# Performance work log

Hardware: AMD Instinct MI355X
Metric: run time of the kernel (lower is better)

The kernel has to match this reference:

```python
import jax, jax.numpy as jnp
import numpy as np

B, N, M, D, H = 2, 2048, 77, 1024, 16
DH = D // H
SCALE = DH ** -0.5
EPS = 1e-5


def _round_ste(x):
    return x + jax.lax.stop_gradient(jnp.round(x) - x)


def _fq(x, delta, zp, n_bits):
    # UniformAffineQuantizer: fake quant-dequant with straight-through round
    xi = _round_ste(x / delta) + zp
    xq = jnp.clip(xi, 0.0, 2.0 ** n_bits - 1.0)
    return (xq - zp) * delta


def _ln(x, g, b):
    mu = jnp.mean(x, -1, keepdims=True)
    var = jnp.var(x, -1, keepdims=True)
    return (x - mu) * jax.lax.rsqrt(var + EPS) * g + b


def _attn(x, ctx, wq, wk, wv, wo, bo, dq, dk, dv, dw):
    b, n, _ = x.shape
    m = ctx.shape[1]
    q = (x @ wq).reshape(b, n, H, DH).transpose(0, 2, 1, 3)   # b h n d
    k = (ctx @ wk).reshape(b, m, H, DH).transpose(0, 2, 1, 3)
    v = (ctx @ wv).reshape(b, m, H, DH).transpose(0, 2, 1, 3)
    sim = jnp.einsum('bhid,bhjd->bhij', _fq(q, dq, 128.0, 8), _fq(k, dk, 128.0, 8)) * SCALE
    attn = jax.nn.softmax(sim, axis=-1)
    out = jnp.einsum('bhij,bhjd->bhid', _fq(attn, dw, 0.0, 8), _fq(v, dv, 128.0, 8))
    out = out.transpose(0, 2, 1, 3).reshape(b, n, D)
    return out @ wo + bo


def setup_inputs():
    key = jax.random.key(0)
    ks = jax.random.split(key, 16)
    w = lambda k, s: (jax.random.normal(k, s, jnp.float32) * 0.02)
    d = lambda v: jnp.full((1,), v, jnp.float32)
    return {
        'x': jax.random.normal(ks[0], (B, N, D), jnp.float32),
        'context': jax.random.normal(ks[1], (B, M, D), jnp.float32),
        'ln1_g': jnp.ones((D,), jnp.float32), 'ln1_b': jnp.zeros((D,), jnp.float32),
        'ln2_g': jnp.ones((D,), jnp.float32), 'ln2_b': jnp.zeros((D,), jnp.float32),
        'ln3_g': jnp.ones((D,), jnp.float32), 'ln3_b': jnp.zeros((D,), jnp.float32),
        'a1_wq': w(ks[2], (D, D)), 'a1_wk': w(ks[3], (D, D)), 'a1_wv': w(ks[4], (D, D)),
        'a1_wo': w(ks[5], (D, D)), 'a1_bo': jnp.zeros((D,), jnp.float32),
        'a2_wq': w(ks[6], (D, D)), 'a2_wk': w(ks[7], (D, D)), 'a2_wv': w(ks[8], (D, D)),
        'a2_wo': w(ks[9], (D, D)), 'a2_bo': jnp.zeros((D,), jnp.float32),
        'ff_w1': w(ks[10], (D, 8 * D)), 'ff_b1': jnp.zeros((8 * D,), jnp.float32),
        'ff_w2': w(ks[11], (4 * D, D)), 'ff_b2': jnp.zeros((D,), jnp.float32),
        'd_q1': d(0.02), 'd_k1': d(0.02), 'd_v1': d(0.02), 'd_w1': d(1.0 / 255.0),
        'd_q2': d(0.02), 'd_k2': d(0.02), 'd_v2': d(0.02), 'd_w2': d(1.0 / 255.0),
    }


def reference(x, context, ln1_g, ln1_b, ln2_g, ln2_b, ln3_g, ln3_b,
              a1_wq, a1_wk, a1_wv, a1_wo, a1_bo,
              a2_wq, a2_wk, a2_wv, a2_wo, a2_bo,
              ff_w1, ff_b1, ff_w2, ff_b2,
              d_q1, d_k1, d_v1, d_w1, d_q2, d_k2, d_v2, d_w2):
    # x = attn1(norm1(x)) + x   (self-attention)
    h1 = _ln(x, ln1_g, ln1_b)
    x = _attn(h1, h1, a1_wq, a1_wk, a1_wv, a1_wo, a1_bo, d_q1, d_k1, d_v1, d_w1) + x
    # x = attn2(norm2(x), context) + x   (cross-attention)
    h2 = _ln(x, ln2_g, ln2_b)
    x = _attn(h2, context, a2_wq, a2_wk, a2_wv, a2_wo, a2_bo, d_q2, d_k2, d_v2, d_w2) + x
    # x = ff(norm3(x)) + x   (GEGLU feed-forward)
    h3 = _ln(x, ln3_g, ln3_b)
    hg = h3 @ ff_w1 + ff_b1
    a, g = jnp.split(hg, 2, axis=-1)
    x = (a * jax.nn.gelu(g, approximate=False)) @ ff_w2 + ff_b2 + x
    return x
```

## Files before the change

### kernel.cpp

```cpp
#include <hip/hip_runtime.h>
#include <cstdint>
#include <cmath>

typedef unsigned short u16;
typedef unsigned int   u32;

typedef __bf16 bx8 __attribute__((ext_vector_type(8)));
typedef float  fx4 __attribute__((ext_vector_type(4)));

#define H_  16
#define DH_ 64
#define QSCALE 0.18033688011112042f

__device__ __forceinline__ float bf2f(u16 h){ return __uint_as_float(((u32)h) << 16); }
__device__ __forceinline__ u16 f2bf(float f){
  u32 u = __float_as_uint(f);
  u32 r = (u + 0x7FFFu + ((u >> 16) & 1u)) >> 16;
  return (u16)r;
}

__device__ __forceinline__ u32 pk_bf16(float a, float b){
  u32 r;
  asm("v_cvt_pk_bf16_f32 %0, %1, %2" : "=v"(r) : "v"(a), "v"(b));
  return r;
}

__device__ __forceinline__ float ldv(const void* p, size_t i, int f32){
  return f32 ? ((const float*)p)[i] : bf2f(((const u16*)p)[i]);
}

__device__ __forceinline__ void gld16(const void* g, void* l){
  __builtin_amdgcn_global_load_lds((const __attribute__((address_space(1))) u32*)g,
                                   (__attribute__((address_space(3))) u32*)l,
                                   16, 0, 0);
}

__device__ __forceinline__ float fq_val(float v, float delta){
  float xi = rintf(v / delta) + 128.0f;
  xi = fminf(fmaxf(xi, 0.0f), 255.0f);
  return (xi - 128.0f) * delta;
}

__device__ __forceinline__ float gelu_f(float x){
  float x3 = x * x * x;
  float z = 0.7978845608028654f * x + 0.035677408136300125f * x3;
  float u = __expf(-2.0f * z);
  float t = 1.0f - 2.0f * u / (1.0f + u);
  return 0.5f * x * (1.0f + t);
}

__global__ void detect_k(const u32* __restrict__ x, int* __restrict__ flag){
  __shared__ int cnt;
  if (threadIdx.x == 0) cnt = 0;
  __syncthreads();
  u32 w = x[threadIdx.x];
  int e = (w >> 7) & 0xFF;
  if (e >= 100 && e <= 140) atomicAdd(&cnt, 1);
  __syncthreads();
  if (threadIdx.x == 0) *flag = (cnt < 192) ? 1 : 0;
}

__global__ __launch_bounds__(256) void cvt_k(const void* __restrict__ in, u16* __restrict__ out,
                                             int n, const int* __restrict__ flagp){
  int f32 = *flagp;
  int i = blockIdx.x * 256 + threadIdx.x;
  if (i < n) out[i] = f32 ? f2bf(((const float*)in)[i]) : ((const u16*)in)[i];
}

__global__ __launch_bounds__(256) void tr8_k(
    const void* s0, const void* s1, const void* s2, const void* s3,
    const void* s4, const void* s5, const void* s6, const void* s7,
    u16* __restrict__ out, const int* __restrict__ flagp){
  __shared__ u16 t[32][33];
  int f32 = *flagp;
  int z = blockIdx.z;
  const void* in = z==0?s0:z==1?s1:z==2?s2:z==3?s3:z==4?s4:z==5?s5:z==6?s6:s7;
  u16* o = out + ((size_t)z << 20);
  int n0 = blockIdx.x << 5, r0 = blockIdx.y << 5;
  int tx = threadIdx.x & 31, ty = threadIdx.x >> 5;
  #pragma unroll
  for (int i = 0; i < 4; i++)
    t[ty + i*8][tx] = f2bf(ldv(in, (size_t)(r0 + ty + i*8) * 1024 + n0 + tx, f32));
  __syncthreads();
  #pragma unroll
  for (int i = 0; i < 4; i++)
    o[(size_t)(n0 + ty + i*8) * 1024 + r0 + tx] = t[tx][ty + i*8];
}

__global__ __launch_bounds__(256) void tr_k(const void* __restrict__ in, u16* __restrict__ out,
                                            int Rout, int C, const int* __restrict__ flagp){
  __shared__ u16 t[32][33];
  int f32 = *flagp;
  int n0 = blockIdx.x << 5, r0 = blockIdx.y << 5;
  int tx = threadIdx.x & 31, ty = threadIdx.x >> 5;
  #pragma unroll
  for (int i = 0; i < 4; i++)
    t[ty + i*8][tx] = f2bf(ldv(in, (size_t)(r0 + ty + i*8) * C + n0 + tx, f32));
  __syncthreads();
  #pragma unroll
  for (int i = 0; i < 4; i++)
    out[(size_t)(n0 + ty + i*8) * Rout + r0 + tx] = t[tx][ty + i*8];
}

__global__ __launch_bounds__(256) void ln_k(const void* __restrict__ x,
    const void* __restrict__ gam, const void* __restrict__ bet, u16* __restrict__ out,
    const int* __restrict__ flagp, int xdual){
  __shared__ float sb[8];
  const int f32 = *flagp;
  const int f32x = xdual ? f32 : 0;
  const int row = blockIdx.x, t = threadIdx.x;
  float v0, v1, v2, v3;
  if (f32x){
    float4 xv = *(const float4*)((const float*)x + (size_t)row * 1024 + t * 4);
    v0 = xv.x; v1 = xv.y; v2 = xv.z; v3 = xv.w;
  } else {
    ushort4 xv = *(const ushort4*)((const u16*)x + (size_t)row * 1024 + t * 4);
    v0 = bf2f(xv.x); v1 = bf2f(xv.y); v2 = bf2f(xv.z); v3 = bf2f(xv.w);
  }
  float s = v0 + v1 + v2 + v3;
  #pragma unroll
  for (int mk = 32; mk; mk >>= 1) s += __shfl_xor(s, mk);
  if ((t & 63) == 0) sb[t >> 6] = s;
  __syncthreads();
  float mu = (sb[0] + sb[1] + sb[2] + sb[3]) * 0.0009765625f;
  float d0 = v0 - mu, d1 = v1 - mu, d2 = v2 - mu, d3 = v3 - mu;
  float ss = d0*d0 + d1*d1 + d2*d2 + d3*d3;
  #pragma unroll
  for (int mk = 32; mk; mk >>= 1) ss += __shfl_xor(ss, mk);
  if ((t & 63) == 0) sb[4 + (t >> 6)] = ss;
  __syncthreads();
  float var = (sb[4] + sb[5] + sb[6] + sb[7]) * 0.0009765625f;
  float rs = rsqrtf(var + 1e-5f);
  int c = t * 4;
  u16 o0 = f2bf(d0 * rs * ldv(gam, c+0, f32) + ldv(bet, c+0, f32));
  u16 o1 = f2bf(d1 * rs * ldv(gam, c+1, f32) + ldv(bet, c+1, f32));
  u16 o2 = f2bf(d2 * rs * ldv(gam, c+2, f32) + ldv(bet, c+2, f32));
  u16 o3 = f2bf(d3 * rs * ldv(gam, c+3, f32) + ldv(bet, c+3, f32));
  uint2 ov; ov.x = (u32)o0 | ((u32)o1 << 16); ov.y = (u32)o2 | ((u32)o3 << 16);
  *(uint2*)(out + (size_t)row * 1024 + c) = ov;
}

__global__ __launch_bounds__(512)
void gemm_mr(const u16* __restrict__ A, const u16* __restrict__ BT,
             u16* __restrict__ P0, u16* __restrict__ P1, u16* __restrict__ P2,
             const void* D0, const void* D1, const void* D2,
             float sc0, float sc1, float sc2,
             int md0, int md1, int md2,
             const int* __restrict__ flagp,
             int M, int K, int rpb, int npad)
{
  __shared__ u16 As[2][128 * 32];
  __shared__ u16 Bs[2][128 * 32];
  const int tid = threadIdx.x;
  const int l = tid & 63, w = tid >> 6;
  const int lr = l & 15, lq = l >> 4;
  const int m0 = blockIdx.y * 128, n0 = blockIdx.x * 128;
  const int wrow = (w & 3) * 32, wcol = (w >> 2) * 64;

  fx4 acc[2][4];
  #pragma unroll
  for (int i = 0; i < 2; i++)
    #pragma unroll
    for (int j = 0; j < 4; j++){ fx4 z = {0.f,0.f,0.f,0.f}; acc[i][j] = z; }

  const int r0 = tid >> 2, p0 = tid & 3;
  const int c0 = p0 ^ (r0 & 3);
  int am0 = m0 + r0; if (am0 > M - 1) am0 = M - 1;
  const u16* gA = A  + (size_t)am0 * K + c0 * 8;
  const u16* gB = BT + (size_t)(n0 + r0) * K + c0 * 8;
  const int lo = w * 512;

  const int nk = K >> 5;
  gld16(gA, &As[0][lo]);
  gld16(gB, &Bs[0][lo]);

  for (int kt = 0; kt < nk; ++kt){
    __syncthreads();
    const int cur = kt & 1;
    if (kt + 1 < nk){
      const int nb = cur ^ 1;
      const int ko = (kt + 1) << 5;
      gld16(gA + ko, &As[nb][lo]);
      gld16(gB + ko, &Bs[nb][lo]);
    }
    bx8 aF[2], bF[4];
    #pragma unroll
    for (int i = 0; i < 2; i++){
      int row = wrow + i * 16 + lr;
      aF[i] = *(const bx8*)&As[cur][row * 32 + (lq ^ (row & 3)) * 8];
    }
    #pragma unroll
    for (int j = 0; j < 4; j++){
      int row = wcol + j * 16 + lr;
      bF[j] = *(const bx8*)&Bs[cur][row * 32 + (lq ^ (row & 3)) * 8];
    }
    #pragma unroll
    for (int i = 0; i < 2; i++)
      #pragma unroll
      for (int j = 0; j < 4; j++)
        acc[i][j] = __builtin_amdgcn_mfma_f32_16x16x32_bf16(aF[i], bF[j], acc[i][j], 0, 0, 0);
  }

  const int f32 = *flagp;
  const int reg = n0 >> 10;
  const int cbase = n0 & 1023;
  u16* P = reg == 0 ? P0 : (reg == 1 ? P1 : P2);
  const void* D = reg == 0 ? D0 : (reg == 1 ? D1 : D2);
  const float sc = reg == 0 ? sc0 : (reg == 1 ? sc1 : sc2);
  const int md = reg == 0 ? md0 : (reg == 1 ? md1 : md2);
  const float delta = ldv(D, 0, f32);

  #pragma unroll
  for (int i = 0; i < 2; i++)
    #pragma unroll
    for (int j = 0; j < 4; j++)
      #pragma unroll
      for (int rr = 0; rr < 4; rr++){
        int gm = m0 + wrow + i * 16 + lq * 4 + rr;
        int col = cbase + wcol + j * 16 + lr;
        if (gm < M){
          float v = fq_val(acc[i][j][rr], delta) * sc;
          if (md == 0){
            P[(size_t)gm * 1024 + col] = f2bf(v);
          } else {
            int bb = gm / rpb; int jj = gm - bb * rpb;
            int hh = col >> 6, dh = col & 63;
            P[(size_t)((bb * H_ + hh) * DH_ + dh) * npad + jj] = f2bf(v);
          }
        }
      }
}

template<int MODE>
__global__ __launch_bounds__(256)
void gemm64(const u16* __restrict__ A, const u16* __restrict__ BT,
            void* __restrict__ Co, const void* __restrict__ res,
            const void* __restrict__ bias, const void* __restrict__ dptr, float sc,
            const int* __restrict__ flagp, int res_dual,
            int M, int K)
{
  __shared__ u16 As[2][64 * 32];
  __shared__ u16 Bs[2][128 * 32];
  const int tid = threadIdx.x;
  const int l = tid & 63, w = tid >> 6;
  const int lr = l & 15, lq = l >> 4;
  const int m0 = blockIdx.y * 64, n0 = blockIdx.x * 128;
  const int wrow = (w >> 1) * 32, wcol = (w & 1) * 64;

  fx4 acc[2][4];
  #pragma unroll
  for (int i = 0; i < 2; i++)
    #pragma unroll
    for (int j = 0; j < 4; j++){ fx4 z = {0.f,0.f,0.f,0.f}; acc[i][j] = z; }

  const int r0 = tid >> 2, p0 = tid & 3;
  const int c0 = p0 ^ (r0 & 3);
  const int r1 = r0 + 64;
  int am0 = m0 + r0; if (am0 > M - 1) am0 = M - 1;
  const u16* gA0 = A  + (size_t)am0 * K + c0 * 8;
  const u16* gB0 = BT + (size_t)(n0 + r0) * K + c0 * 8;
  const u16* gB1 = BT + (size_t)(n0 + r1) * K + c0 * 8;
  const int lo0 = (w * 64) * 8, lo1 = (256 + w * 64) * 8;

  const int nk = K >> 5;
  gld16(gA0, &As[0][lo0]);
  gld16(gB0, &Bs[0][lo0]);
  gld16(gB1, &Bs[0][lo1]);

  for (int kt = 0; kt < nk; ++kt){
    __syncthreads();
    const int cur = kt & 1;
    if (kt + 1 < nk){
      const int nb = cur ^ 1;
      const int ko = (kt + 1) << 5;
      gld16(gA0 + ko, &As[nb][lo0]);
      gld16(gB0 + ko, &Bs[nb][lo0]);
      gld16(gB1 + ko, &Bs[nb][lo1]);
    }
    bx8 aF[2], bF[4];
    #pragma unroll
    for (int i = 0; i < 2; i++){
      int row = wrow + i * 16 + lr;
      aF[i] = *(const bx8*)&As[cur][row * 32 + (lq ^ (row & 3)) * 8];
    }
    #pragma unroll
    for (int j = 0; j < 4; j++){
      int row = wcol + j * 16 + lr;
      bF[j] = *(const bx8*)&Bs[cur][row * 32 + (lq ^ (row & 3)) * 8];
    }
    #pragma unroll
    for (int i = 0; i < 2; i++)
      #pragma unroll
      for (int j = 0; j < 4; j++)
        acc[i][j] = __builtin_amdgcn_mfma_f32_16x16x32_bf16(aF[i], bF[j], acc[i][j], 0, 0, 0);
  }

  const int f32 = *flagp;
  float delta = 1.f;
  if (MODE == 0) delta = ldv(dptr, 0, f32);

  #pragma unroll
  for (int i = 0; i < 2; i++)
    #pragma unroll
    for (int j = 0; j < 4; j++)
      #pragma unroll
      for (int rr = 0; rr < 4; rr++){
        int gm = m0 + wrow + i * 16 + lq * 4 + rr;
        int gn = n0 + wcol + j * 16 + lr;
        if (gm < M){
          float v = acc[i][j][rr];
          size_t idx = (size_t)gm * 1024 + gn;
          if (MODE == 0){
            ((u16*)Co)[idx] = f2bf(fq_val(v, delta) * sc);
          } else if (MODE == 5){
            float r = res_dual ? ldv(res, idx, f32) : bf2f(((const u16*)res)[idx]);
            ((u16*)Co)[idx] = f2bf(v + ldv(bias, gn, f32) + r);
          } else {
            float o = v + ldv(bias, gn, f32) + bf2f(((const u16*)res)[idx]);
            if (f32) ((float*)Co)[idx] = o;
            else     ((u16*)Co)[idx]  = f2bf(o);
          }
        }
      }
}

__global__ __launch_bounds__(512)
void gemm_glu(const u16* __restrict__ A, const u16* __restrict__ WT,
              u16* __restrict__ GE, const void* __restrict__ bias,
              const int* __restrict__ flagp, int M, int K)
{
  __shared__ u16 As[2][128 * 32];
  __shared__ u16 Ba[2][128 * 32];
  __shared__ u16 Bg[2][128 * 32];
  const int tid = threadIdx.x;
  const int l = tid & 63, w = tid >> 6;
  const int lr = l & 15, lq = l >> 4;
  const int m0 = blockIdx.y * 128, n0 = blockIdx.x * 128;
  const int wrow = (w & 3) * 32, wcol = (w >> 2) * 64;

  fx4 accA[2][4], accG[2][4];
  #pragma unroll
  for (int i = 0; i < 2; i++)
    #pragma unroll
    for (int j = 0; j < 4; j++){
      fx4 z = {0.f,0.f,0.f,0.f}; accA[i][j] = z; accG[i][j] = z;
    }

  const int r0 = tid >> 2, p0 = tid & 3;
  const int c0 = p0 ^ (r0 & 3);
  int am0 = m0 + r0; if (am0 > M - 1) am0 = M - 1;
  const u16* gA  = A  + (size_t)am0 * K + c0 * 8;
  const u16* gBa = WT + (size_t)(n0 + r0) * K + c0 * 8;
  const u16* gBg = WT + (size_t)(4096 + n0 + r0) * K + c0 * 8;
  const int lo = w * 512;

  const int nk = K >> 5;
  gld16(gA,  &As[0][lo]);
  gld16(gBa, &Ba[0][lo]);
  gld16(gBg, &Bg[0][lo]);

  for (int kt = 0; kt < nk; ++kt){
    __syncthreads();
    const int cur = kt & 1;
    if (kt + 1 < nk){
      const int nb = cur ^ 1;
      const int ko = (kt + 1) << 5;
      gld16(gA + ko,  &As[nb][lo]);
      gld16(gBa + ko, &Ba[nb][lo]);
      gld16(gBg + ko, &Bg[nb][lo]);
    }
    bx8 aF[2], bFa[4], bFg[4];
    #pragma unroll
    for (int i = 0; i < 2; i++){
      int row = wrow + i * 16 + lr;
      aF[i] = *(const bx8*)&As[cur][row * 32 + (lq ^ (row & 3)) * 8];
    }
    #pragma unroll
    for (int j = 0; j < 4; j++){
      int row = wcol + j * 16 + lr;
      bFa[j] = *(const bx8*)&Ba[cur][row * 32 + (lq ^ (row & 3)) * 8];
      bFg[j] = *(const bx8*)&Bg[cur][row * 32 + (lq ^ (row & 3)) * 8];
    }
    #pragma unroll
    for (int i = 0; i < 2; i++)
      #pragma unroll
      for (int j = 0; j < 4; j++){
        accA[i][j] = __builtin_amdgcn_mfma_f32_16x16x32_bf16(aF[i], bFa[j], accA[i][j], 0, 0, 0);
        accG[i][j] = __builtin_amdgcn_mfma_f32_16x16x32_bf16(aF[i], bFg[j], accG[i][j], 0, 0, 0);
      }
  }

  const int f32 = *flagp;

  #pragma unroll
  for (int i = 0; i < 2; i++)
    #pragma unroll
    for (int j = 0; j < 4; j++)
      #pragma unroll
      for (int rr = 0; rr < 4; rr++){
        int gm = m0 + wrow + i * 16 + lq * 4 + rr;
        int gn = n0 + wcol + j * 16 + lr;
        float va = accA[i][j][rr] + ldv(bias, gn, f32);
        float vg = accG[i][j][rr] + ldv(bias, 4096 + gn, f32);
        GE[(size_t)gm * 4096 + gn] = f2bf(va * gelu_f(vg));
      }
}

__global__ __launch_bounds__(512, 4) void attn_k(
    const u16* __restrict__ Qf, const u16* __restrict__ Kf,
    const u16* __restrict__ VT, u16* __restrict__ AO,
    const void* __restrict__ dwp, const int* __restrict__ flagp,
    int Nq, int Lk, int Lpad)
{
  __shared__ u16 lds[40960];
  u16* const KB0 = lds;
  u16* const KB1 = lds + 8192;
  u16* const Vs  = lds + 16384;
  u16* const Ps  = lds + 24576;

  const int tid = threadIdx.x, l = tid & 63, w = tid >> 6;
  const int lr = l & 15, lq = l >> 4, m = lr & 7;
  const int q0 = blockIdx.x << 7;
  const int b = blockIdx.y >> 4, hh = blockIdx.y & 15;
  const int wq = w << 4;
  const float dw = ldv(dwp, 0, *flagp);

  const u16* qp = Qf + ((size_t)(b * Nq + q0 + wq + lr) << 10) + (hh << 6) + (lq << 3);
  bx8 aQ0 = *(const bx8*)(qp);
  bx8 aQ1 = *(const bx8*)(qp + 32);

  const int krl = (w << 3) + (l >> 3), kcl = l & 7;
  const int vrl = (w << 2) + (l >> 4), vcl = l & 15;

  auto stageK = [&](u16* dst, int j0){
    #pragma unroll
    for (int t = 0; t < 2; ++t){
      int r = krl + (t << 6);
      int jr = j0 + r; if (jr > Lk - 1) jr = Lk - 1;
      int c = kcl ^ (r & 7);
      gld16(Kf + ((size_t)(b * Lk + jr) << 10) + (hh << 6) + (c << 3),
            dst + (w << 9) + (t << 12));
    }
  };
  auto stageV = [&](int j0){
    #pragma unroll
    for (int t = 0; t < 2; ++t){
      int dh = vrl + (t << 5);
      int c = vcl ^ (dh & 7);
      gld16(VT + (size_t)((((b << 4) + hh) << 6) + dh) * Lpad + j0 + (c << 3),
            Vs + (w << 9) + (t << 12));
    }
  };

  const int ntiles = (Lk + 127) >> 7;
  const int ch0 = ((lq ^ m) << 3), ch1 = (((lq + 4) ^ m) << 3);

  float sa0 = 0.f, sa1 = 0.f, sa2 = 0.f, sa3 = 0.f;
  stageK(KB0, 0);
  for (int jt = 0; jt < ntiles; ++jt){
    __syncthreads();
    const u16* Kc = (jt & 1) ? KB1 : KB0;
    if (jt + 1 < ntiles) stageK((jt & 1) ? KB0 : KB1, (jt + 1) << 7);
    const int j0 = jt << 7;
    const bool full = (j0 + 128 <= Lk);
    #pragma unroll
    for (int j = 0; j < 8; ++j){
      const int ro = ((j << 4) + lr) << 6;
      bx8 k0 = *(const bx8*)&Kc[ro + ch0];
      bx8 k1 = *(const bx8*)&Kc[ro + ch1];
      fx4 sv = {0.f,0.f,0.f,0.f};
      sv = __builtin_amdgcn_mfma_f32_16x16x32_bf16(k0, aQ0, sv, 0, 0, 0);
      sv = __builtin_amdgcn_mfma_f32_16x16x32_bf16(k1, aQ1, sv, 0, 0, 0);
      if (full){
        sa0 += exp2f(sv[0]); sa1 += exp2f(sv[1]);
        sa2 += exp2f(sv[2]); sa3 += exp2f(sv[3]);
      } else {
        const int kb = j0 + (j << 4) + (lq << 2);
        sa0 += (kb + 0 < Lk) ? exp2f(sv[0]) : 0.f;
        sa1 += (kb + 1 < Lk) ? exp2f(sv[1]) : 0.f;
        sa2 += (kb + 2 < Lk) ? exp2f(sv[2]) : 0.f;
        sa3 += (kb + 3 < Lk) ? exp2f(sv[3]) : 0.f;
      }
    }
  }
  __syncthreads();
  float s = (sa0 + sa1) + (sa2 + sa3);
  s += __shfl_xor(s, 16);
  s += __shfl_xor(s, 32);
  const float cr = (1.0f / dw) / s;

  fx4 oacc[4];
  #pragma unroll
  for (int dj = 0; dj < 4; ++dj){ fx4 z = {0.f,0.f,0.f,0.f}; oacc[dj] = z; }

  const int qloc = wq + lr;
  const int pw = (qloc << 7) + (lq << 2);

  stageK(KB0, 0);
  for (int jt = 0; jt < ntiles; ++jt){
    __syncthreads();
    const int j0 = jt << 7;
    stageV(j0);
    if (jt + 1 < ntiles) stageK((jt & 1) ? KB0 : KB1, j0 + 128);
    const u16* Kc = (jt & 1) ? KB1 : KB0;
    const bool full = (j0 + 128 <= Lk);
    #pragma unroll
    for (int j = 0; j < 8; ++j){
      const int ro = ((j << 4) + lr) << 6;
      bx8 k0 = *(const bx8*)&Kc[ro + ch0];
      bx8 k1 = *(const bx8*)&Kc[ro + ch1];
      fx4 sv = {0.f,0.f,0.f,0.f};
      sv = __builtin_amdgcn_mfma_f32_16x16x32_bf16(k0, aQ0, sv, 0, 0, 0);
      sv = __builtin_amdgcn_mfma_f32_16x16x32_bf16(k1, aQ1, sv, 0, 0, 0);
      float x0, x1, x2, x3;
      if (full){
        x0 = rintf(exp2f(sv[0]) * cr);
        x1 = rintf(exp2f(sv[1]) * cr);
        x2 = rintf(exp2f(sv[2]) * cr);
        x3 = rintf(exp2f(sv[3]) * cr);
      } else {
        const int kb = j0 + (j << 4) + (lq << 2);
        x0 = (kb + 0 < Lk) ? rintf(exp2f(sv[0]) * cr) : 0.f;
        x1 = (kb + 1 < Lk) ? rintf(exp2f(sv[1]) * cr) : 0.f;
        x2 = (kb + 2 < Lk) ? rintf(exp2f(sv[2]) * cr) : 0.f;
        x3 = (kb + 3 < Lk) ? rintf(exp2f(sv[3]) * cr) : 0.f;
      }
      uint2 pp; pp.x = pk_bf16(x0, x1); pp.y = pk_bf16(x2, x3);
      *(uint2*)&Ps[pw + ((j ^ m) << 4)] = pp;
    }
    __syncthreads();
    #pragma unroll
    for (int kk = 0; kk < 4; ++kk){
      bx8 aP = *(const bx8*)&Ps[(qloc << 7) + ((((kk << 3) + (lq << 1)) ^ (m << 2)) << 2)];
      #pragma unroll
      for (int dj = 0; dj < 4; ++dj){
        bx8 bV = *(const bx8*)&Vs[((((dj << 4) + lr)) << 7) + ((((kk << 2) + lq) ^ m) << 3)];
        oacc[dj] = __builtin_amdgcn_mfma_f32_16x16x32_bf16(aP, bV, oacc[dj], 0, 0, 0);
      }
    }
  }

  const size_t ob = ((size_t)(b * Nq + q0 + wq + (lq << 2)) << 10) + (hh << 6) + lr;
  #pragma unroll
  for (int dj = 0; dj < 4; ++dj)
    #pragma unroll
    for (int rr = 0; rr < 4; ++rr)
      AO[ob + ((size_t)rr << 10) + (dj << 4)] = f2bf(oacc[dj][rr] * dw);
}


extern "C" void kernel_launch(void* const* d_in, const int* in_sizes, int n_in,
                              void* d_out, int out_size, void* d_ws, size_t ws_size,
                              hipStream_t stream)
{
  const void* X    = d_in[0];
  const void* CTX  = d_in[1];
  const void* LN1G = d_in[2];
  const void* LN1B = d_in[3];
  const void* LN2G = d_in[4];
  const void* LN2B = d_in[5];
  const void* LN3G = d_in[6];
  const void* LN3B = d_in[7];
  const void* W1Q  = d_in[8];
  const void* W1K  = d_in[9];
  const void* W1V  = d_in[10];
  const void* W1O  = d_in[11];
  const void* B1O  = d_in[12];
  const void* W2Q  = d_in[13];
  const void* W2K  = d_in[14];
  const void* W2V  = d_in[15];
  const void* W2O  = d_in[16];
  const void* B2O  = d_in[17];
  const void* FW1  = d_in[18];
  const void* FB1  = d_in[19];
  const void* FW2  = d_in[20];
  const void* FB2  = d_in[21];
  const void* DQ1  = d_in[22];
  const void* DK1  = d_in[23];
  const void* DV1  = d_in[24];
  const void* DW1  = d_in[25];
  const void* DQ2  = d_in[26];
  const void* DK2  = d_in[27];
  const void* DV2  = d_in[28];
  const void* DW2  = d_in[29];

  char* ws = (char*)d_ws;
  u16* wslot = (u16*)(ws + (0ull  << 20));
  u16* xs    = (u16*)(ws + (16ull << 20));
  u16* h     = (u16*)(ws + (24ull << 20));
  u16* bufA  = (u16*)(ws + (32ull << 20));
  u16* bufB  = (u16*)(ws + (40ull << 20));
  u16* bufC  = (u16*)(ws + (48ull << 20));
  u16* ge    = bufA;
  u16* ctxc  = (u16*)(ws + (64ull << 20));
  int* flag  = (int*)(ws + (65ull << 20));

  const dim3 G8x64(8, 64), GAT(16, 32);
  const int NCTX = 154 * 1024;
  const size_t MB2 = 1048576;

  detect_k<<<1, 256, 0, stream>>>((const u32*)X, flag);
  cvt_k<<<(NCTX + 255) / 256, 256, 0, stream>>>(CTX, ctxc, NCTX, flag);
  tr8_k<<<dim3(32, 32, 8), 256, 0, stream>>>(W1Q, W1K, W1V, W1O, W2Q, W2K, W2V, W2O,
                                             wslot, flag);

  ln_k<<<4096, 256, 0, stream>>>(X, LN1G, LN1B, h, flag, 1);
  gemm_mr<<<dim3(24, 32), 512, 0, stream>>>(h, wslot,
      bufA, bufB, bufC, DQ1, DK1, DV1, QSCALE, 1.f, 1.f, 0, 0, 1,
      flag, 4096, 1024, 2048, 2048);
  attn_k<<<GAT, 512, 0, stream>>>(bufA, bufB, bufC, h, DW1, flag, 2048, 2048, 2048);
  gemm64<5><<<G8x64, 256, 0, stream>>>(h, wslot + 3 * MB2, xs, X, B1O, nullptr, 1.f,
                                       flag, 1, 4096, 1024);

  ln_k<<<4096, 256, 0, stream>>>(xs, LN2G, LN2B, h, flag, 0);
  gemm64<0><<<G8x64, 256, 0, stream>>>(h, wslot + 4 * MB2, bufA, nullptr, nullptr, DQ2,
                                       QSCALE, flag, 0, 4096, 1024);
  gemm_mr<<<dim3(16, 2), 512, 0, stream>>>(ctxc, wslot + 5 * MB2,
      bufB, bufC, nullptr, DK2, DV2, DV2, 1.f, 1.f, 1.f, 0, 1, 1,
      flag, 154, 1024, 77, 128);
  attn_k<<<GAT, 512, 0, stream>>>(bufA, bufB, bufC, h, DW2, flag, 2048, 77, 128);
  gemm64<5><<<G8x64, 256, 0, stream>>>(h, wslot + 7 * MB2, xs, xs, B2O, nullptr, 1.f,
                                       flag, 0, 4096, 1024);

  ln_k<<<4096, 256, 0, stream>>>(xs, LN3G, LN3B, h, flag, 0);
  tr_k<<<dim3(256, 32), 256, 0, stream>>>(FW1, wslot, 1024, 8192, flag);
  gemm_glu<<<dim3(32, 32), 512, 0, stream>>>(h, wslot, ge, FB1, flag, 4096, 1024);
  tr_k<<<dim3(32, 128), 256, 0, stream>>>(FW2, wslot, 4096, 1024, flag);
  gemm64<7><<<G8x64, 256, 0, stream>>>(ge, wslot, d_out, xs, FB2, nullptr, 1.f,
                                       flag, 0, 4096, 4096);
}
```

Baseline: 659.2 us.

## Restructure attention kernel: 4 waves with 32 query rows, register P via permlane

The attention kernel now runs 256 threads per block, and each wave handles two 16-row query groups. Each K fragment loaded from LDS is therefore reused across two MFMA chains. The P matrix no longer goes through an LDS round trip and barrier: the accumulators are computed transposed and repacked in registers with permlane swap instructions. V is also double-buffered alongside K, which removes the mid-tile barrier, and exp2 uses the hardware intrinsic. This costs more registers per wave and lowers the wave count per block, which may reduce latency hiding.

```diff
diff --git a/kernel.cpp b/kernel.cpp
--- a/kernel.cpp
+++ b/kernel.cpp
@@ -7,10 +7,17 @@
 
 typedef __bf16 bx8 __attribute__((ext_vector_type(8)));
 typedef float  fx4 __attribute__((ext_vector_type(4)));
+typedef u32    ux4 __attribute__((ext_vector_type(4)));
 
 #define H_  16
 #define DH_ 64
 #define QSCALE 0.18033688011112042f
+
+#if __has_builtin(__builtin_amdgcn_exp2f)
+#define EXP2(x) __builtin_amdgcn_exp2f(x)
+#else
+#define EXP2(x) exp2f(x)
+#endif
 
 __device__ __forceinline__ float bf2f(u16 h){ return __uint_as_float(((u32)h) << 16); }
 __device__ __forceinline__ u16 f2bf(float f){
@@ -24,6 +31,8 @@
   asm("v_cvt_pk_bf16_f32 %0, %1, %2" : "=v"(r) : "v"(a), "v"(b));
   return r;
 }
+
+union pkc { ux4 u; bx8 v; };
 
 __device__ __forceinline__ float ldv(const void* p, size_t i, int f32){
   return f32 ? ((const float*)p)[i] : bf2f(((const u16*)p)[i]);
@@ -406,61 +415,72 @@
       }
 }
 
-__global__ __launch_bounds__(512, 4) void attn_k(
+__global__ __launch_bounds__(256) void attn_k(
     const u16* __restrict__ Qf, const u16* __restrict__ Kf,
     const u16* __restrict__ VT, u16* __restrict__ AO,
     const void* __restrict__ dwp, const int* __restrict__ flagp,
     int Nq, int Lk, int Lpad)
 {
-  __shared__ u16 lds[40960];
-  u16* const KB0 = lds;
-  u16* const KB1 = lds + 8192;
-  u16* const Vs  = lds + 16384;
-  u16* const Ps  = lds + 24576;
+  __shared__ u16 lds[32768];
+  u16* const KB0_ = lds;
+  u16* const KB1_ = lds + 8192;
+  u16* const VB0_ = lds + 16384;
+  u16* const VB1_ = lds + 24576;
 
   const int tid = threadIdx.x, l = tid & 63, w = tid >> 6;
   const int lr = l & 15, lq = l >> 4, m = lr & 7;
   const int q0 = blockIdx.x << 7;
   const int b = blockIdx.y >> 4, hh = blockIdx.y & 15;
-  const int wq = w << 4;
+  const int wq = w << 5;
   const float dw = ldv(dwp, 0, *flagp);
-
-  const u16* qp = Qf + ((size_t)(b * Nq + q0 + wq + lr) << 10) + (hh << 6) + (lq << 3);
-  bx8 aQ0 = *(const bx8*)(qp);
-  bx8 aQ1 = *(const bx8*)(qp + 32);
-
-  const int krl = (w << 3) + (l >> 3), kcl = l & 7;
-  const int vrl = (w << 2) + (l >> 4), vcl = l & 15;
+  const float rdw = 1.0f / dw;
+
+  bx8 aQ[2][2];
+  #pragma unroll
+  for (int g = 0; g < 2; ++g){
+    const u16* qp = Qf + ((size_t)(b * Nq + q0 + wq + g * 16 + lr) << 10)
+                       + (hh << 6) + (lq << 3);
+    aQ[g][0] = *(const bx8*)(qp);
+    aQ[g][1] = *(const bx8*)(qp + 32);
+  }
+
+  const int kr0 = tid >> 3, kc = (tid & 7) ^ (kr0 & 7);
+  const int vd0 = tid >> 4, vc = (tid & 15) ^ (vd0 & 7);
+  const int ldsb = w << 9;
 
   auto stageK = [&](u16* dst, int j0){
     #pragma unroll
-    for (int t = 0; t < 2; ++t){
-      int r = krl + (t << 6);
+    for (int q = 0; q < 4; ++q){
+      int r = kr0 + (q << 5);
       int jr = j0 + r; if (jr > Lk - 1) jr = Lk - 1;
-      int c = kcl ^ (r & 7);
-      gld16(Kf + ((size_t)(b * Lk + jr) << 10) + (hh << 6) + (c << 3),
-            dst + (w << 9) + (t << 12));
+      gld16(Kf + ((size_t)(b * Lk + jr) << 10) + (hh << 6) + (kc << 3),
+            dst + (q << 11) + ldsb);
     }
   };
-  auto stageV = [&](int j0){
-    #pragma unroll
-    for (int t = 0; t < 2; ++t){
-      int dh = vrl + (t << 5);
-      int c = vcl ^ (dh & 7);
-      gld16(VT + (size_t)((((b << 4) + hh) << 6) + dh) * Lpad + j0 + (c << 3),
-            Vs + (w << 9) + (t << 12));
+  auto stageV = [&](u16* dst, int j0){
+    #pragma unroll
+    for (int q = 0; q < 4; ++q){
+      int d = vd0 + (q << 4);
+      gld16(VT + ((size_t)(((b << 4) + hh) << 6) + d) * Lpad + j0 + (vc << 3),
+            dst + (q << 11) + ldsb);
     }
   };
 
   const int ntiles = (Lk + 127) >> 7;
   const int ch0 = ((lq ^ m) << 3), ch1 = (((lq + 4) ^ m) << 3);
 
-  float sa0 = 0.f, sa1 = 0.f, sa2 = 0.f, sa3 = 0.f;
-  stageK(KB0, 0);
+  float sa[2][4];
+  #pragma unroll
+  for (int g = 0; g < 2; ++g)
+    #pragma unroll
+    for (int rr = 0; rr < 4; ++rr) sa[g][rr] = 0.f;
+
+  stageK(KB0_, 0);
   for (int jt = 0; jt < ntiles; ++jt){
     __syncthreads();
-    const u16* Kc = (jt & 1) ? KB1 : KB0;
-    if (jt + 1 < ntiles) stageK((jt & 1) ? KB0 : KB1, (jt + 1) << 7);
+    const int cur = jt & 1;
+    if (jt + 1 < ntiles) stageK(cur ? KB0_ : KB1_, (jt + 1) << 7);
+    const u16* Kc = cur ? KB1_ : KB0_;
     const int j0 = jt << 7;
     const bool full = (j0 + 128 <= Lk);
     #pragma unroll
@@ -468,84 +488,117 @@
       const int ro = ((j << 4) + lr) << 6;
       bx8 k0 = *(const bx8*)&Kc[ro + ch0];
       bx8 k1 = *(const bx8*)&Kc[ro + ch1];
-      fx4 sv = {0.f,0.f,0.f,0.f};
-      sv = __builtin_amdgcn_mfma_f32_16x16x32_bf16(k0, aQ0, sv, 0, 0, 0);
-      sv = __builtin_amdgcn_mfma_f32_16x16x32_bf16(k1, aQ1, sv, 0, 0, 0);
-      if (full){
-        sa0 += exp2f(sv[0]); sa1 += exp2f(sv[1]);
-        sa2 += exp2f(sv[2]); sa3 += exp2f(sv[3]);
-      } else {
-        const int kb = j0 + (j << 4) + (lq << 2);
-        sa0 += (kb + 0 < Lk) ? exp2f(sv[0]) : 0.f;
-        sa1 += (kb + 1 < Lk) ? exp2f(sv[1]) : 0.f;
-        sa2 += (kb + 2 < Lk) ? exp2f(sv[2]) : 0.f;
-        sa3 += (kb + 3 < Lk) ? exp2f(sv[3]) : 0.f;
-      }
-    }
-  }
+      #pragma unroll
+      for (int g = 0; g < 2; ++g){
+        fx4 sv = {0.f,0.f,0.f,0.f};
+        sv = __builtin_amdgcn_mfma_f32_16x16x32_bf16(k0, aQ[g][0], sv, 0, 0, 0);
+        sv = __builtin_amdgcn_mfma_f32_16x16x32_bf16(k1, aQ[g][1], sv, 0, 0, 0);
+        if (full){
+          sa[g][0] += EXP2(sv[0]); sa[g][1] += EXP2(sv[1]);
+          sa[g][2] += EXP2(sv[2]); sa[g][3] += EXP2(sv[3]);
+        } else {
+          const int kb = j0 + (j << 4) + (lq << 2);
+          sa[g][0] += (kb + 0 < Lk) ? EXP2(sv[0]) : 0.f;
+          sa[g][1] += (kb + 1 < Lk) ? EXP2(sv[1]) : 0.f;
+          sa[g][2] += (kb + 2 < Lk) ? EXP2(sv[2]) : 0.f;
+          sa[g][3] += (kb + 3 < Lk) ? EXP2(sv[3]) : 0.f;
+        }
+      }
+    }
+  }
+
+  float cr[2];
+  #pragma unroll
+  for (int g = 0; g < 2; ++g){
+    float s = (sa[g][0] + sa[g][1]) + (sa[g][2] + sa[g][3]);
+    s += __shfl_xor(s, 16);
+    s += __shfl_xor(s, 32);
+    cr[g] = rdw / s;
+  }
+
+  fx4 oacc[2][4];
+  #pragma unroll
+  for (int g = 0; g < 2; ++g)
+    #pragma unroll
+    for (int dj = 0; dj < 4; ++dj){ fx4 z = {0.f,0.f,0.f,0.f}; oacc[g][dj] = z; }
+
   __syncthreads();
-  float s = (sa0 + sa1) + (sa2 + sa3);
-  s += __shfl_xor(s, 16);
-  s += __shfl_xor(s, 32);
-  const float cr = (1.0f / dw) / s;
-
-  fx4 oacc[4];
-  #pragma unroll
-  for (int dj = 0; dj < 4; ++dj){ fx4 z = {0.f,0.f,0.f,0.f}; oacc[dj] = z; }
-
-  const int qloc = wq + lr;
-  const int pw = (qloc << 7) + (lq << 2);
-
-  stageK(KB0, 0);
+  stageK(KB0_, 0);
+  stageV(VB0_, 0);
   for (int jt = 0; jt < ntiles; ++jt){
     __syncthreads();
+    const int cur = jt & 1;
     const int j0 = jt << 7;
-    stageV(j0);
-    if (jt + 1 < ntiles) stageK((jt & 1) ? KB0 : KB1, j0 + 128);
-    const u16* Kc = (jt & 1) ? KB1 : KB0;
+    if (jt + 1 < ntiles){
+      stageK(cur ? KB0_ : KB1_, j0 + 128);
+      stageV(cur ? VB0_ : VB1_, j0 + 128);
+    }
+    const u16* Kc = cur ? KB1_ : KB0_;
+    const u16* Vc = cur ? VB1_ : VB0_;
     const bool full = (j0 + 128 <= Lk);
     #pragma unroll
-    for (int j = 0; j < 8; ++j){
-      const int ro = ((j << 4) + lr) << 6;
-      bx8 k0 = *(const bx8*)&Kc[ro + ch0];
-      bx8 k1 = *(const bx8*)&Kc[ro + ch1];
-      fx4 sv = {0.f,0.f,0.f,0.f};
-      sv = __builtin_amdgcn_mfma_f32_16x16x32_bf16(k0, aQ0, sv, 0, 0, 0);
-      sv = __builtin_amdgcn_mfma_f32_16x16x32_bf16(k1, aQ1, sv, 0, 0, 0);
-      float x0, x1, x2, x3;
-      if (full){
-        x0 = rintf(exp2f(sv[0]) * cr);
-        x1 = rintf(exp2f(sv[1]) * cr);
-        x2 = rintf(exp2f(sv[2]) * cr);
-        x3 = rintf(exp2f(sv[3]) * cr);
-      } else {
-        const int kb = j0 + (j << 4) + (lq << 2);
-        x0 = (kb + 0 < Lk) ? rintf(exp2f(sv[0]) * cr) : 0.f;
-        x1 = (kb + 1 < Lk) ? rintf(exp2f(sv[1]) * cr) : 0.f;
-        x2 = (kb + 2 < Lk) ? rintf(exp2f(sv[2]) * cr) : 0.f;
-        x3 = (kb + 3 < Lk) ? rintf(exp2f(sv[3]) * cr) : 0.f;
-      }
-      uint2 pp; pp.x = pk_bf16(x0, x1); pp.y = pk_bf16(x2, x3);
-      *(uint2*)&Ps[pw + ((j ^ m) << 4)] = pp;
-    }
-    __syncthreads();
-    #pragma unroll
-    for (int kk = 0; kk < 4; ++kk){
-      bx8 aP = *(const bx8*)&Ps[(qloc << 7) + ((((kk << 3) + (lq << 1)) ^ (m << 2)) << 2)];
+    for (int t = 0; t < 4; ++t){
+      u32 pA0[2], pA1[2], pB0[2], pB1[2];
+      #pragma unroll
+      for (int jj = 0; jj < 2; ++jj){
+        const int j = (t << 1) + jj;
+        const int ro = ((j << 4) + lr) << 6;
+        bx8 k0 = *(const bx8*)&Kc[ro + ch0];
+        bx8 k1 = *(const bx8*)&Kc[ro + ch1];
+        #pragma unroll
+        for (int g = 0; g < 2; ++g){
+          fx4 sv = {0.f,0.f,0.f,0.f};
+          sv = __builtin_amdgcn_mfma_f32_16x16x32_bf16(k0, aQ[g][0], sv, 0, 0, 0);
+          sv = __builtin_amdgcn_mfma_f32_16x16x32_bf16(k1, aQ[g][1], sv, 0, 0, 0);
+          float x0, x1, x2, x3;
+          if (full){
+            x0 = rintf(EXP2(sv[0]) * cr[g]);
+            x1 = rintf(EXP2(sv[1]) * cr[g]);
+            x2 = rintf(EXP2(sv[2]) * cr[g]);
+            x3 = rintf(EXP2(sv[3]) * cr[g]);
+          } else {
+            const int kb = j0 + (j << 4) + (lq << 2);
+            x0 = (kb + 0 < Lk) ? rintf(EXP2(sv[0]) * cr[g]) : 0.f;
+            x1 = (kb + 1 < Lk) ? rintf(EXP2(sv[1]) * cr[g]) : 0.f;
+            x2 = (kb + 2 < Lk) ? rintf(EXP2(sv[2]) * cr[g]) : 0.f;
+            x3 = (kb + 3 < Lk) ? rintf(EXP2(sv[3]) * cr[g]) : 0.f;
+          }
+          u32 plo = pk_bf16(x0, x1), phi = pk_bf16(x2, x3);
+          if (jj == 0){ pA0[g] = plo; pA1[g] = phi; }
+          else        { pB0[g] = plo; pB1[g] = phi; }
+        }
+      }
+      bx8 pa[2];
+      #pragma unroll
+      for (int g = 0; g < 2; ++g){
+        u32 r0 = pA0[g], r2 = pB0[g], r1 = pA1[g], r3 = pB1[g];
+        asm volatile("v_permlane32_swap_b32 %0, %1" : "+v"(r0), "+v"(r2));
+        asm volatile("v_permlane16_swap_b32 %0, %1" : "+v"(r0), "+v"(r2));
+        asm volatile("v_permlane32_swap_b32 %0, %1" : "+v"(r1), "+v"(r3));
+        asm volatile("v_permlane16_swap_b32 %0, %1" : "+v"(r1), "+v"(r3));
+        pkc pc; ux4 uu = {r0, r1, r2, r3}; pc.u = uu; pa[g] = pc.v;
+      }
       #pragma unroll
       for (int dj = 0; dj < 4; ++dj){
-        bx8 bV = *(const bx8*)&Vs[((((dj << 4) + lr)) << 7) + ((((kk << 2) + lq) ^ m) << 3)];
-        oacc[dj] = __builtin_amdgcn_mfma_f32_16x16x32_bf16(aP, bV, oacc[dj], 0, 0, 0);
-      }
-    }
-  }
-
-  const size_t ob = ((size_t)(b * Nq + q0 + wq + (lq << 2)) << 10) + (hh << 6) + lr;
-  #pragma unroll
-  for (int dj = 0; dj < 4; ++dj)
-    #pragma unroll
-    for (int rr = 0; rr < 4; ++rr)
-      AO[ob + ((size_t)rr << 10) + (dj << 4)] = f2bf(oacc[dj][rr] * dw);
+        bx8 bV = *(const bx8*)&Vc[(((dj << 4) + lr) << 7) + ((((t << 2) + lq) ^ m) << 3)];
+        oacc[0][dj] = __builtin_amdgcn_mfma_f32_16x16x32_bf16(bV, pa[0], oacc[0][dj], 0, 0, 0);
+        oacc[1][dj] = __builtin_amdgcn_mfma_f32_16x16x32_bf16(bV, pa[1], oacc[1][dj], 0, 0, 0);
+      }
+    }
+  }
+
+  #pragma unroll
+  for (int g = 0; g < 2; ++g){
+    const size_t ob = ((size_t)(b * Nq + q0 + wq + g * 16 + lr) << 10)
+                    + (hh << 6) + (lq << 2);
+    #pragma unroll
+    for (int dj = 0; dj < 4; ++dj){
+      uint2 ov;
+      ov.x = (u32)f2bf(oacc[g][dj][0] * dw) | ((u32)f2bf(oacc[g][dj][1] * dw) << 16);
+      ov.y = (u32)f2bf(oacc[g][dj][2] * dw) | ((u32)f2bf(oacc[g][dj][3] * dw) << 16);
+      *(uint2*)(AO + ob + (dj << 4)) = ov;
+    }
+  }
 }
 
 
@@ -608,7 +661,7 @@
   gemm_mr<<<dim3(24, 32), 512, 0, stream>>>(h, wslot,
       bufA, bufB, bufC, DQ1, DK1, DV1, QSCALE, 1.f, 1.f, 0, 0, 1,
       flag, 4096, 1024, 2048, 2048);
-  attn_k<<<GAT, 512, 0, stream>>>(bufA, bufB, bufC, h, DW1, flag, 2048, 2048, 2048);
+  attn_k<<<GAT, 256, 0, stream>>>(bufA, bufB, bufC, h, DW1, flag, 2048, 2048, 2048);
   gemm64<5><<<G8x64, 256, 0, stream>>>(h, wslot + 3 * MB2, xs, X, B1O, nullptr, 1.f,
                                        flag, 1, 4096, 1024);
 
@@ -618,7 +671,7 @@
   gemm_mr<<<dim3(16, 2), 512, 0, stream>>>(ctxc, wslot + 5 * MB2,
       bufB, bufC, nullptr, DK2, DV2, DV2, 1.f, 1.f, 1.f, 0, 1, 1,
       flag, 154, 1024, 77, 128);
-  attn_k<<<GAT, 512, 0, stream>>>(bufA, bufB, bufC, h, DW2, flag, 2048, 77, 128);
+  attn_k<<<GAT, 256, 0, stream>>>(bufA, bufB, bufC, h, DW2, flag, 2048, 77, 128);
   gemm64<5><<<G8x64, 256, 0, stream>>>(h, wslot + 7 * MB2, xs, xs, B2O, nullptr, 1.f,
                                        flag, 0, 4096, 1024);
 
```

Result: no change. 651.1 us (-1.2%).
